# Optimization experiments

Hardware: AMD Instinct MI355X
Metric: run time of the kernel (lower is better)

## Reference

```python
import jax, jax.numpy as jnp
import numpy as np

EMBED = 384
HEADS = 6
HEAD_SIZE = EMBED // HEADS
EPS = 1e-5


def _layernorm(x, g, b):
    mu = jnp.mean(x, axis=-1, keepdims=True)
    var = jnp.mean(jnp.square(x - mu), axis=-1, keepdims=True)
    return (x - mu) * jax.lax.rsqrt(var + EPS) * g + b


def setup_inputs() -> dict:
    key = jax.random.key(0)
    ks = jax.random.split(key, 16)
    B, T = 64, 256
    s_in = 1.0 / np.sqrt(EMBED)
    return {
        "x": jax.random.normal(ks[0], (B, T, EMBED), dtype=jnp.float32),
        # per-head q/k/v projections, stacked over heads: [H, C, D]
        "Wq": jax.random.normal(ks[1], (HEADS, EMBED, HEAD_SIZE), dtype=jnp.float32) * s_in,
        "bq": jnp.zeros((HEADS, HEAD_SIZE), dtype=jnp.float32),
        "Wk": jax.random.normal(ks[2], (HEADS, EMBED, HEAD_SIZE), dtype=jnp.float32) * s_in,
        "bk": jnp.zeros((HEADS, HEAD_SIZE), dtype=jnp.float32),
        "Wv": jax.random.normal(ks[3], (HEADS, EMBED, HEAD_SIZE), dtype=jnp.float32) * s_in,
        "bv": jnp.zeros((HEADS, HEAD_SIZE), dtype=jnp.float32),
        "Wp": jax.random.normal(ks[4], (EMBED, EMBED), dtype=jnp.float32) * s_in,
        "bp": jnp.zeros((EMBED,), dtype=jnp.float32),
        "W1": jax.random.normal(ks[5], (EMBED, EMBED), dtype=jnp.float32) * s_in,
        "b1": jnp.zeros((EMBED,), dtype=jnp.float32),
        "W2": jax.random.normal(ks[6], (EMBED, EMBED), dtype=jnp.float32) * s_in,
        "b2": jnp.zeros((EMBED,), dtype=jnp.float32),
        "ln1_g": jnp.ones((EMBED,), dtype=jnp.float32),
        "ln1_b": jnp.zeros((EMBED,), dtype=jnp.float32),
        "ln2_g": jnp.ones((EMBED,), dtype=jnp.float32),
        "ln2_b": jnp.zeros((EMBED,), dtype=jnp.float32),
    }


def reference(x, Wq, bq, Wk, bk, Wv, bv, Wp, bp, W1, b1, W2, b2,
              ln1_g, ln1_b, ln2_g, ln2_b):
    B, T, C = x.shape
    h = _layernorm(x, ln1_g, ln1_b)
    # batched per-head projections: [B,H,T,D]
    q = jnp.einsum('btc,hcd->bhtd', h, Wq) + bq[None, :, None, :]
    k = jnp.einsum('btc,hcd->bhtd', h, Wk) + bk[None, :, None, :]
    v = jnp.einsum('btc,hcd->bhtd', h, Wv) + bv[None, :, None, :]
    # NOTE: original scales by embed_size**0.5 (C=384), not head_size.
    wei = jnp.einsum('bhtd,bhsd->bhts', q, k) / jnp.sqrt(jnp.float32(C))
    causal = jnp.tril(jnp.ones((T, T), dtype=bool))
    wei = jnp.where(causal[None, None], wei, -jnp.inf)
    wei = jax.nn.softmax(wei, axis=-1)  # dropout = identity in eval
    attn = jnp.einsum('bhts,bhsd->bhtd', wei, v)  # [B,H,T,D]
    # concat heads in head order -> [B,T,C]
    attn = attn.transpose(0, 2, 1, 3).reshape(B, T, C)
    x = x + attn @ Wp + bp
    h2 = _layernorm(x, ln2_g, ln2_b)
    ff = jax.nn.relu(h2 @ W1 + b1) @ W2 + b2
    return x + ff
```

## Files before the change

kernel.cpp:

```cpp
#include <hip/hip_runtime.h>

typedef _Float16 f16;
typedef _Float16 half8 __attribute__((ext_vector_type(8)));
typedef _Float16 half4v __attribute__((ext_vector_type(4)));
typedef float floatx4 __attribute__((ext_vector_type(4)));

#define B_ 64
#define T_ 256
#define C_ 384
#define H_ 6
#define D_ 64
#define NROWS (B_*T_)

typedef __attribute__((address_space(3))) void lds_void_t;
typedef const __attribute__((address_space(1))) void gvoid_t;

__device__ __forceinline__ void g2lds16(const void* g, void* l) {
  __builtin_amdgcn_global_load_lds((gvoid_t*)g, (lds_void_t*)l, 16, 0, 0);
}

__global__ __launch_bounds__(256) void prep_ln_kernel(
    const float* __restrict__ Wq, const float* __restrict__ Wk, const float* __restrict__ Wv,
    const float* __restrict__ bq, const float* __restrict__ bk, const float* __restrict__ bv,
    const float* __restrict__ Wp, const float* __restrict__ W1, const float* __restrict__ W2,
    f16* __restrict__ Wqkv_t, f16* __restrict__ Wp_t, f16* __restrict__ W1_t, f16* __restrict__ W2_t,
    float* __restrict__ bqkv,
    const float* __restrict__ x, const float* __restrict__ gamma, const float* __restrict__ beta,
    f16* __restrict__ hout)
{
  const int bid = blockIdx.x;
  const int tid = threadIdx.x;
  if (bid >= 217) {
    int row = (bid - 217) * 4 + (tid >> 6);
    int lane = tid & 63;
    const float* xr = x + (size_t)row * 384;
    float v[6]; float s = 0.f;
#pragma unroll
    for (int j = 0; j < 6; j++) { v[j] = xr[lane + 64*j]; s += v[j]; }
#pragma unroll
    for (int m = 1; m < 64; m <<= 1) s += __shfl_xor(s, m);
    float mu = s * (1.f/384.f);
    float var = 0.f;
#pragma unroll
    for (int j = 0; j < 6; j++) { float d = v[j]-mu; var += d*d; }
#pragma unroll
    for (int m = 1; m < 64; m <<= 1) var += __shfl_xor(var, m);
    float rs = rsqrtf(var * (1.f/384.f) + 1e-5f);
    f16* orow = hout + (size_t)row*384;
#pragma unroll
    for (int j = 0; j < 6; j++) {
      int col = lane + 64*j;
      orow[col] = (f16)((v[j]-mu)*rs*gamma[col] + beta[col]);
    }
    return;
  }
  if (bid == 216) {
    for (int i = tid; i < 1152; i += 256) {
      float v;
      if (i < 384)      v = bq[i];
      else if (i < 768) v = bk[i - 384];
      else              v = bv[i - 768];
      bqkv[i] = v;
    }
    return;
  }
  __shared__ __align__(16) float tile[64*68];
  const float* src; int srcStride; f16* dst;
  if (bid < 108) {
    int mat = bid / 36, rem = bid - mat*36;
    int h = rem / 6, kt = rem - h*6;
    const float* W = (mat == 0) ? Wq : (mat == 1) ? Wk : Wv;
    src = W + (size_t)(h*384 + kt*64)*64;
    srcStride = 64;
    dst = Wqkv_t + (size_t)(mat*384 + h*64)*384 + kt*64;
  } else {
    int b2 = bid - 108;
    int mat = b2 / 36, rem = b2 - mat*36;
    int kt = rem / 6, ct = rem - kt*6;
    const float* W = (mat == 0) ? Wp : (mat == 1) ? W1 : W2;
    src = W + (size_t)(kt*64)*384 + ct*64;
    srcStride = 384;
    f16* O = (mat == 0) ? Wp_t : (mat == 1) ? W1_t : W2_t;
    dst = O + (size_t)(ct*64)*384 + kt*64;
  }
#pragma unroll
  for (int i = 0; i < 4; i++) {
    int idx = i*256 + tid;
    int r = idx >> 4, c4 = idx & 15;
    float4 v = *(const float4*)(src + (size_t)r*srcStride + c4*4);
    *(float4*)(&tile[r*68 + c4*4]) = v;
  }
  __syncthreads();
#pragma unroll
  for (int i = 0; i < 4; i++) {
    int idx = i*256 + tid;
    int d = idx >> 4, k4 = idx & 15;
    half4v o;
#pragma unroll
    for (int j = 0; j < 4; j++) o[j] = (f16)tile[(k4*4 + j)*68 + d];
    *(half4v*)(dst + (size_t)d*384 + k4*4) = o;
  }
}

__global__ __launch_bounds__(256) void ln_kernel(const float* __restrict__ x,
    const float* __restrict__ gamma, const float* __restrict__ beta, f16* __restrict__ out)
{
  int row = blockIdx.x * 4 + (threadIdx.x >> 6);
  int lane = threadIdx.x & 63;
  const float* xr = x + (size_t)row * 384;
  float v[6]; float s = 0.f;
#pragma unroll
  for (int j = 0; j < 6; j++) { v[j] = xr[lane + 64*j]; s += v[j]; }
#pragma unroll
  for (int m = 1; m < 64; m <<= 1) s += __shfl_xor(s, m);
  float mu = s * (1.f/384.f);
  float var = 0.f;
#pragma unroll
  for (int j = 0; j < 6; j++) { float d = v[j]-mu; var += d*d; }
#pragma unroll
  for (int m = 1; m < 64; m <<= 1) var += __shfl_xor(var, m);
  float rs = rsqrtf(var * (1.f/384.f) + 1e-5f);
  f16* orow = out + (size_t)row*384;
#pragma unroll
  for (int j = 0; j < 6; j++) {
    int col = lane + 64*j;
    orow[col] = (f16)((v[j]-mu)*rs*gamma[col] + beta[col]);
  }
}

template<int MODE>
__global__ __launch_bounds__(256) void gemm_kernel(
    const f16* __restrict__ A, const f16* __restrict__ Bt,
    const float* __restrict__ bias, const float* __restrict__ res,
    void* __restrict__ outp, int ldo)
{
  __shared__ __align__(16) f16 As[2][128*32];
  __shared__ __align__(16) f16 Bs[2][128*32];
  const int tid = threadIdx.x;
  const int lane = tid & 63, w = tid >> 6;
  const int wm = w >> 1, wn = w & 1;
  const int q = lane >> 4, c15 = lane & 15;
  const long row0 = (long)blockIdx.x * 128;
  const long col0 = (long)blockIdx.y * 128;
  floatx4 acc[4][4] = {};

  const int c0 = tid,        r0c = c0 >> 2, p0 = c0 & 3, g0 = p0 ^ ((r0c >> 1) & 3);
  const int c1 = 256 + tid,  r1c = c1 >> 2, p1 = c1 & 3, g1 = p1 ^ ((r1c >> 1) & 3);
  const f16* Arow0 = A  + (row0 + r0c)*384 + g0*8;
  const f16* Arow1 = A  + (row0 + r1c)*384 + g1*8;
  const f16* Brow0 = Bt + (col0 + r0c)*384 + g0*8;
  const f16* Brow1 = Bt + (col0 + r1c)*384 + g1*8;
  const int dof0 = (w*64)*8, dof1 = (256 + w*64)*8;

  for (int k0 = 0; k0 < 384; k0 += 64) {
#pragma unroll
    for (int hf = 0; hf < 2; hf++) {
      int kk = k0 + hf*32;
      g2lds16(Arow0 + kk, &As[hf][dof0]);
      g2lds16(Arow1 + kk, &As[hf][dof1]);
      g2lds16(Brow0 + kk, &Bs[hf][dof0]);
      g2lds16(Brow1 + kk, &Bs[hf][dof1]);
    }
    __syncthreads();
#pragma unroll
    for (int hf = 0; hf < 2; hf++) {
      half8 af[4], bf[4];
#pragma unroll
      for (int mi = 0; mi < 4; mi++) {
        int r = wm*64 + mi*16 + c15;
        int ph = q ^ ((r >> 1) & 3);
        af[mi] = *(const half8*)(&As[hf][r*32 + ph*8]);
      }
#pragma unroll
      for (int ni = 0; ni < 4; ni++) {
        int r = wn*64 + ni*16 + c15;
        int ph = q ^ ((r >> 1) & 3);
        bf[ni] = *(const half8*)(&Bs[hf][r*32 + ph*8]);
      }
#pragma unroll
      for (int mi = 0; mi < 4; mi++)
#pragma unroll
        for (int ni = 0; ni < 4; ni++)
          acc[mi][ni] = __builtin_amdgcn_mfma_f32_16x16x32_f16(af[mi], bf[ni], acc[mi][ni], 0, 0, 0);
    }
    __syncthreads();
  }

#pragma unroll
  for (int ni = 0; ni < 4; ni++) {
    long col = col0 + wn*64 + ni*16 + c15;
    float bv = bias[col];
#pragma unroll
    for (int mi = 0; mi < 4; mi++) {
      long rowb = row0 + wm*64 + mi*16 + q*4;
#pragma unroll
      for (int r = 0; r < 4; r++) {
        float vo = acc[mi][ni][r] + bv;
        if (MODE == 1) vo = vo > 0.f ? vo : 0.f;
        long o = (rowb + r) * (long)ldo + col;
        if (MODE == 2) {
          ((float*)outp)[o] = vo + res[o];
        } else {
          ((f16*)outp)[o] = (f16)vo;
        }
      }
    }
  }
}

__global__ __launch_bounds__(256, 3) void attn_kernel(const f16* __restrict__ qkv,
                                                      f16* __restrict__ attn_out)
{
  __shared__ __align__(16) char kvbuf[32768];
  __shared__ __align__(16) f16 Pbuf[4][16*128];
  f16* Ks = (f16*)kvbuf;
  unsigned int* vTw = (unsigned int*)kvbuf;
  f16* vT = (f16*)kvbuf;

  const int tid = threadIdx.x;
  const int bid = blockIdx.x;
  const int bh = bid >> 2, qt = bid & 3;
  const int b = bh / 6, h = bh - b*6;
  const f16* qp = qkv + (size_t)b*256*1152 + h*64;
  const f16* kp = qp + 384;
  const f16* vp = qp + 768;
  const int lane = tid & 63, w = tid >> 6;
  const int q = lane >> 4, c15 = lane & 15;

  {
    const int iters = (qt + 1) * 2;
    const int pcbase = w*64 + lane;
    for (int i = 0; i < iters; i++) {
      int pc = i*256 + pcbase;
      int rc = pc >> 3, p = pc & 7;
      int c = p ^ (rc & 7);
      g2lds16(kp + (size_t)rc*1152 + c*8, (char*)kvbuf + (size_t)(i*256 + w*64)*16);
    }
  }
  __syncthreads();

  const int nmax = qt*4 + w;
  const int trow0 = qt*64 + w*16;
  const f16* qrow = qp + (size_t)(trow0 + c15)*1152 + q*8;
  half8 aq0 = *(const half8*)(qrow);
  half8 aq1 = *(const half8*)(qrow + 32);

  floatx4 sacc[16];
#pragma unroll
  for (int ni = 0; ni < 16; ni++) {
    if (ni <= nmax) {
      int s = ni*16 + c15;
      const f16* kr = Ks + s*64;
      int p0 = q ^ (s & 7);
      half8 b0 = *(const half8*)(kr + p0*8);
      half8 b1 = *(const half8*)(kr + (p0 ^ 4)*8);
      floatx4 a = {0.f, 0.f, 0.f, 0.f};
      a = __builtin_amdgcn_mfma_f32_16x16x32_f16(aq0, b0, a, 0, 0, 0);
      a = __builtin_amdgcn_mfma_f32_16x16x32_f16(aq1, b1, a, 0, 0, 0);
      sacc[ni] = a;
    }
  }

  const float scale = 0.051031036307982884f;
  float mx[4] = {-1e30f, -1e30f, -1e30f, -1e30f};
#pragma unroll
  for (int ni = 0; ni < 16; ni++) {
    if (ni < nmax) {
#pragma unroll
      for (int r = 0; r < 4; r++) { float v = sacc[ni][r]*scale; sacc[ni][r] = v; mx[r] = fmaxf(mx[r], v); }
    } else if (ni == nmax) {
#pragma unroll
      for (int r = 0; r < 4; r++) {
        float v = sacc[ni][r]*scale;
        v = (c15 <= q*4 + r) ? v : -1e30f;
        sacc[ni][r] = v; mx[r] = fmaxf(mx[r], v);
      }
    }
  }
#pragma unroll
  for (int r = 0; r < 4; r++) {
    mx[r] = fmaxf(mx[r], __shfl_xor(mx[r], 1));
    mx[r] = fmaxf(mx[r], __shfl_xor(mx[r], 2));
    mx[r] = fmaxf(mx[r], __shfl_xor(mx[r], 4));
    mx[r] = fmaxf(mx[r], __shfl_xor(mx[r], 8));
  }
  float l[4] = {0.f, 0.f, 0.f, 0.f};
#pragma unroll
  for (int ni = 0; ni < 16; ni++) {
    if (ni <= nmax) {
#pragma unroll
      for (int r = 0; r < 4; r++) { float p = __expf(sacc[ni][r] - mx[r]); sacc[ni][r] = p; l[r] += p; }
    }
  }
#pragma unroll
  for (int r = 0; r < 4; r++) {
    l[r] += __shfl_xor(l[r], 1);
    l[r] += __shfl_xor(l[r], 2);
    l[r] += __shfl_xor(l[r], 4);
    l[r] += __shfl_xor(l[r], 8);
  }
  __syncthreads();

  {
    const int iters = qt + 1;
    for (int i = 0; i < iters; i++) {
      int idx = i*256 + tid;
      int sp = idx >> 3, part = idx & 7;
      const f16* v0 = vp + (size_t)(2*sp)*1152 + part*8;
      half8 va = *(const half8*)(v0);
      half8 vb = *(const half8*)(v0 + 1152);
      int csp = sp >> 2, spw = sp & 3;
#pragma unroll
      for (int j = 0; j < 8; j++) {
        int d = part*8 + j;
        int swz = (d & 15) ^ (d >> 3);
        int p = csp ^ swz;
        union { struct { f16 lo, hi; } s; unsigned int u; } pk;
        pk.s.lo = va[j]; pk.s.hi = vb[j];
        vTw[d*128 + p*4 + spw] = pk.u;
      }
    }
  }
  __syncthreads();

  f16* Pw = &Pbuf[w][0];
  floatx4 oacc[4] = {};
  const int kend_w = (nmax + 1) * 16;
#pragma unroll
  for (int ch = 0; ch < 2; ch++) {
    if (ch*128 < kend_w) {
#pragma unroll
      for (int nl = 0; nl < 8; nl++) {
        int ni = ch*8 + nl;
        if (ni <= nmax) {
#pragma unroll
          for (int r = 0; r < 4; r++) {
            int row = q*4 + r;
            int colp = nl*16 + c15;
            int php = (colp >> 3) ^ row;
            Pw[row*128 + php*8 + (colp & 7)] = (f16)sacc[ni][r];
          }
        } else if (ni == nmax + 1) {
#pragma unroll
          for (int r = 0; r < 4; r++) {
            int row = q*4 + r;
            int colp = nl*16 + c15;
            int php = (colp >> 3) ^ row;
            Pw[row*128 + php*8 + (colp & 7)] = (f16)0.f;
          }
        }
      }
#pragma unroll
      for (int kc = 0; kc < 4; kc++) {
        if (ch*128 + kc*32 < kend_w) {
          int pc = (kc*4 + q) ^ c15;
          half8 ap = *(const half8*)(Pw + c15*128 + pc*8);
          int sc = ch*16 + kc*4 + q;
#pragma unroll
          for (int nt = 0; nt < 4; nt++) {
            int d = nt*16 + c15;
            int swz = (d & 15) ^ (d >> 3);
            half8 bv = *(const half8*)(vT + d*256 + ((sc ^ swz))*8);
            oacc[nt] = __builtin_amdgcn_mfma_f32_16x16x32_f16(ap, bv, oacc[nt], 0, 0, 0);
          }
        }
      }
    }
  }

#pragma unroll
  for (int nt = 0; nt < 4; nt++) {
#pragma unroll
    for (int r = 0; r < 4; r++) {
      int t = trow0 + q*4 + r;
      int d = nt*16 + c15;
      attn_out[(size_t)(b*256 + t)*384 + h*64 + d] = (f16)(oacc[nt][r] / l[r]);
    }
  }
}

extern "C" void kernel_launch(void* const* d_in, const int* in_sizes, int n_in,
                              void* d_out, int out_size, void* d_ws, size_t ws_size,
                              hipStream_t stream) {
  const float* x   = (const float*)d_in[0];
  const float* Wq  = (const float*)d_in[1];
  const float* bq  = (const float*)d_in[2];
  const float* Wk  = (const float*)d_in[3];
  const float* bk  = (const float*)d_in[4];
  const float* Wv  = (const float*)d_in[5];
  const float* bv  = (const float*)d_in[6];
  const float* Wp  = (const float*)d_in[7];
  const float* bp  = (const float*)d_in[8];
  const float* W1  = (const float*)d_in[9];
  const float* b1  = (const float*)d_in[10];
  const float* W2  = (const float*)d_in[11];
  const float* b2  = (const float*)d_in[12];
  const float* g1  = (const float*)d_in[13];
  const float* be1 = (const float*)d_in[14];
  const float* g2  = (const float*)d_in[15];
  const float* be2 = (const float*)d_in[16];

  char* ws = (char*)d_ws;
  size_t off = 0;
  auto alloc = [&](size_t bytes) -> void* {
    void* p = ws + off;
    off += (bytes + 255) & ~(size_t)255;
    return p;
  };
  f16*   Wqkv_t = (f16*)  alloc(1152*384*sizeof(f16));
  f16*   Wp_t   = (f16*)  alloc(384*384*sizeof(f16));
  f16*   W1_t   = (f16*)  alloc(384*384*sizeof(f16));
  f16*   W2_t   = (f16*)  alloc(384*384*sizeof(f16));
  float* bqkv   = (float*)alloc(1152*sizeof(float));
  f16*   h      = (f16*)  alloc((size_t)NROWS*384*sizeof(f16));
  f16*   qkv    = (f16*)  alloc((size_t)NROWS*1152*sizeof(f16));
  f16*   attnb  = (f16*)  alloc((size_t)NROWS*384*sizeof(f16));
  float* x2     = (float*)alloc((size_t)NROWS*384*sizeof(float));
  f16*   h2     = (f16*)  alloc((size_t)NROWS*384*sizeof(f16));
  f16*   mid    = (f16*)  alloc((size_t)NROWS*384*sizeof(f16));

  prep_ln_kernel<<<217 + NROWS/4, 256, 0, stream>>>(Wq, Wk, Wv, bq, bk, bv, Wp, W1, W2,
                                                    Wqkv_t, Wp_t, W1_t, W2_t, bqkv,
                                                    x, g1, be1, h);
  gemm_kernel<0><<<dim3(128, 9), 256, 0, stream>>>(h, Wqkv_t, bqkv, nullptr, qkv, 1152);
  attn_kernel<<<B_*H_*4, 256, 0, stream>>>(qkv, attnb);
  gemm_kernel<2><<<dim3(128, 3), 256, 0, stream>>>(attnb, Wp_t, bp, x, x2, 384);
  ln_kernel<<<NROWS/4, 256, 0, stream>>>(x2, g2, be2, h2);
  gemm_kernel<1><<<dim3(128, 3), 256, 0, stream>>>(h2, W1_t, b1, nullptr, mid, 384);
  gemm_kernel<2><<<dim3(128, 3), 256, 0, stream>>>(mid, W2_t, b2, x2, (float*)d_out, 384);
}
```

Before: 204.6 us.

## Fuse output projection with LayerNorm2 and fuse both FFN GEMMs via LDS

Replaces the separate projection GEMM, LN kernel and two FFN GEMMs with two kernels that each own full 64x384 row tiles. The projection kernel adds bias and residual, then computes LayerNorm in registers. The FFN kernel keeps the ReLU intermediate in LDS and feeds it straight into the second GEMM. This removes the round trips of mid and x2 through global memory plus two launches. In exchange, only 256 blocks run, one per CU by launch bounds, each with large LDS use and a big accumulator array, so occupancy and latency hiding drop and the B tiles are reloaded per block.

Result: slower. 220.5 us (+7.8%).

```diff
diff --git a/kernel.cpp b/kernel.cpp
--- a/kernel.cpp
+++ b/kernel.cpp
@@ -102,37 +102,9 @@
   }
 }
 
-__global__ __launch_bounds__(256) void ln_kernel(const float* __restrict__ x,
-    const float* __restrict__ gamma, const float* __restrict__ beta, f16* __restrict__ out)
-{
-  int row = blockIdx.x * 4 + (threadIdx.x >> 6);
-  int lane = threadIdx.x & 63;
-  const float* xr = x + (size_t)row * 384;
-  float v[6]; float s = 0.f;
-#pragma unroll
-  for (int j = 0; j < 6; j++) { v[j] = xr[lane + 64*j]; s += v[j]; }
-#pragma unroll
-  for (int m = 1; m < 64; m <<= 1) s += __shfl_xor(s, m);
-  float mu = s * (1.f/384.f);
-  float var = 0.f;
-#pragma unroll
-  for (int j = 0; j < 6; j++) { float d = v[j]-mu; var += d*d; }
-#pragma unroll
-  for (int m = 1; m < 64; m <<= 1) var += __shfl_xor(var, m);
-  float rs = rsqrtf(var * (1.f/384.f) + 1e-5f);
-  f16* orow = out + (size_t)row*384;
-#pragma unroll
-  for (int j = 0; j < 6; j++) {
-    int col = lane + 64*j;
-    orow[col] = (f16)((v[j]-mu)*rs*gamma[col] + beta[col]);
-  }
-}
-
-template<int MODE>
-__global__ __launch_bounds__(256) void gemm_kernel(
+__global__ __launch_bounds__(256) void gemm_qkv_kernel(
     const f16* __restrict__ A, const f16* __restrict__ Bt,
-    const float* __restrict__ bias, const float* __restrict__ res,
-    void* __restrict__ outp, int ldo)
+    const float* __restrict__ bias, f16* __restrict__ outp, int ldo)
 {
   __shared__ __align__(16) f16 As[2][128*32];
   __shared__ __align__(16) f16 Bs[2][128*32];
@@ -195,15 +167,210 @@
       long rowb = row0 + wm*64 + mi*16 + q*4;
 #pragma unroll
       for (int r = 0; r < 4; r++) {
-        float vo = acc[mi][ni][r] + bv;
-        if (MODE == 1) vo = vo > 0.f ? vo : 0.f;
-        long o = (rowb + r) * (long)ldo + col;
-        if (MODE == 2) {
-          ((float*)outp)[o] = vo + res[o];
-        } else {
-          ((f16*)outp)[o] = (f16)vo;
+        outp[(rowb + r) * (long)ldo + col] = (f16)(acc[mi][ni][r] + bv);
+      }
+    }
+  }
+}
+
+__global__ __launch_bounds__(256, 1) void projln_kernel(
+    const f16* __restrict__ A, const f16* __restrict__ Bt, const float* __restrict__ bias,
+    const float* __restrict__ res, const float* __restrict__ g2v, const float* __restrict__ be2,
+    float* __restrict__ x2, f16* __restrict__ h2)
+{
+  __shared__ __align__(16) f16 As2[2][64*32];
+  __shared__ __align__(16) f16 Bs2[2][384*32];
+  const int tid = threadIdx.x;
+  const int lane = tid & 63, w = tid >> 6;
+  const int q = lane >> 4, c15 = lane & 15;
+  const long row0 = (long)blockIdx.x * 64;
+  floatx4 acc[24] = {};
+
+  const int rcA = tid >> 2, pA = tid & 3, gA = pA ^ ((rcA >> 1) & 3);
+  const f16* Asrc = A + (row0 + rcA)*384 + gA*8;
+
+  for (int k0 = 0; k0 < 384; k0 += 64) {
+#pragma unroll
+    for (int hf = 0; hf < 2; hf++) {
+      int kk = k0 + hf*32;
+      g2lds16(Asrc + kk, &As2[hf][(w*64)*8]);
+#pragma unroll
+      for (int i = 0; i < 6; i++) {
+        int pc = i*256 + tid;
+        int rcB = pc >> 2, pB = pc & 3, gB = pB ^ ((rcB >> 1) & 3);
+        g2lds16(Bt + (size_t)rcB*384 + kk + gB*8, &Bs2[hf][(i*256 + w*64)*8]);
+      }
+    }
+    __syncthreads();
+#pragma unroll
+    for (int hf = 0; hf < 2; hf++) {
+      int ra = w*16 + c15;
+      int pha = q ^ ((ra >> 1) & 3);
+      half8 af = *(const half8*)(&As2[hf][ra*32 + pha*8]);
+#pragma unroll
+      for (int nt = 0; nt < 24; nt++) {
+        int rb = nt*16 + c15;
+        int phb = q ^ ((rb >> 1) & 3);
+        half8 bf = *(const half8*)(&Bs2[hf][rb*32 + phb*8]);
+        acc[nt] = __builtin_amdgcn_mfma_f32_16x16x32_f16(af, bf, acc[nt], 0, 0, 0);
+      }
+    }
+    __syncthreads();
+  }
+
+  const long rowg = row0 + w*16 + q*4;
+#pragma unroll
+  for (int nt = 0; nt < 24; nt++) {
+    int col = nt*16 + c15;
+    float bv = bias[col];
+#pragma unroll
+    for (int r = 0; r < 4; r++) {
+      float v = acc[nt][r] + bv + res[(rowg + r)*384 + col];
+      acc[nt][r] = v;
+      x2[(rowg + r)*384 + col] = v;
+    }
+  }
+  float s[4] = {0.f, 0.f, 0.f, 0.f};
+#pragma unroll
+  for (int nt = 0; nt < 24; nt++)
+#pragma unroll
+    for (int r = 0; r < 4; r++) s[r] += acc[nt][r];
+#pragma unroll
+  for (int r = 0; r < 4; r++) {
+    s[r] += __shfl_xor(s[r], 1);
+    s[r] += __shfl_xor(s[r], 2);
+    s[r] += __shfl_xor(s[r], 4);
+    s[r] += __shfl_xor(s[r], 8);
+  }
+  float mu[4], vs[4] = {0.f, 0.f, 0.f, 0.f};
+#pragma unroll
+  for (int r = 0; r < 4; r++) mu[r] = s[r] * (1.f/384.f);
+#pragma unroll
+  for (int nt = 0; nt < 24; nt++)
+#pragma unroll
+    for (int r = 0; r < 4; r++) { float d = acc[nt][r] - mu[r]; vs[r] += d*d; }
+#pragma unroll
+  for (int r = 0; r < 4; r++) {
+    vs[r] += __shfl_xor(vs[r], 1);
+    vs[r] += __shfl_xor(vs[r], 2);
+    vs[r] += __shfl_xor(vs[r], 4);
+    vs[r] += __shfl_xor(vs[r], 8);
+  }
+  float rs[4];
+#pragma unroll
+  for (int r = 0; r < 4; r++) rs[r] = rsqrtf(vs[r] * (1.f/384.f) + 1e-5f);
+#pragma unroll
+  for (int nt = 0; nt < 24; nt++) {
+    int col = nt*16 + c15;
+    float gg = g2v[col], bb = be2[col];
+#pragma unroll
+    for (int r = 0; r < 4; r++) {
+      h2[(rowg + r)*384 + col] = (f16)((acc[nt][r] - mu[r])*rs[r]*gg + bb);
+    }
+  }
+}
+
+__global__ __launch_bounds__(256, 1) void ffn_kernel(
+    const f16* __restrict__ h2, const f16* __restrict__ W1t, const float* __restrict__ b1,
+    const f16* __restrict__ W2t, const float* __restrict__ b2,
+    const float* __restrict__ x2, float* __restrict__ outp)
+{
+  __shared__ __align__(16) f16 As2[2][64*32];
+  __shared__ __align__(16) f16 Bs2[2][384*32];
+  __shared__ __align__(16) f16 midb[64*384];
+  const int tid = threadIdx.x;
+  const int lane = tid & 63, w = tid >> 6;
+  const int q = lane >> 4, c15 = lane & 15;
+  const long row0 = (long)blockIdx.x * 64;
+
+  const int rcA = tid >> 2, pA = tid & 3, gA = pA ^ ((rcA >> 1) & 3);
+  const f16* Asrc = h2 + (row0 + rcA)*384 + gA*8;
+
+  {
+    floatx4 acc[24] = {};
+    for (int k0 = 0; k0 < 384; k0 += 64) {
+#pragma unroll
+      for (int hf = 0; hf < 2; hf++) {
+        int kk = k0 + hf*32;
+        g2lds16(Asrc + kk, &As2[hf][(w*64)*8]);
+#pragma unroll
+        for (int i = 0; i < 6; i++) {
+          int pc = i*256 + tid;
+          int rcB = pc >> 2, pB = pc & 3, gB = pB ^ ((rcB >> 1) & 3);
+          g2lds16(W1t + (size_t)rcB*384 + kk + gB*8, &Bs2[hf][(i*256 + w*64)*8]);
         }
       }
+      __syncthreads();
+#pragma unroll
+      for (int hf = 0; hf < 2; hf++) {
+        int ra = w*16 + c15;
+        int pha = q ^ ((ra >> 1) & 3);
+        half8 af = *(const half8*)(&As2[hf][ra*32 + pha*8]);
+#pragma unroll
+        for (int nt = 0; nt < 24; nt++) {
+          int rb = nt*16 + c15;
+          int phb = q ^ ((rb >> 1) & 3);
+          half8 bf = *(const half8*)(&Bs2[hf][rb*32 + phb*8]);
+          acc[nt] = __builtin_amdgcn_mfma_f32_16x16x32_f16(af, bf, acc[nt], 0, 0, 0);
+        }
+      }
+      __syncthreads();
+    }
+#pragma unroll
+    for (int nt = 0; nt < 24; nt++) {
+      int col = nt*16 + c15;
+      float bv = b1[col];
+#pragma unroll
+      for (int r = 0; r < 4; r++) {
+        float v = acc[nt][r] + bv;
+        v = v > 0.f ? v : 0.f;
+        int row = w*16 + q*4 + r;
+        int chunk = col >> 3;
+        int ph = chunk ^ (row & 7);
+        midb[row*384 + ph*8 + (col & 7)] = (f16)v;
+      }
+    }
+  }
+  __syncthreads();
+
+  floatx4 acc2[24] = {};
+  for (int k0 = 0; k0 < 384; k0 += 64) {
+#pragma unroll
+    for (int hf = 0; hf < 2; hf++) {
+      int kk = k0 + hf*32;
+#pragma unroll
+      for (int i = 0; i < 6; i++) {
+        int pc = i*256 + tid;
+        int rcB = pc >> 2, pB = pc & 3, gB = pB ^ ((rcB >> 1) & 3);
+        g2lds16(W2t + (size_t)rcB*384 + kk + gB*8, &Bs2[hf][(i*256 + w*64)*8]);
+      }
+    }
+    __syncthreads();
+#pragma unroll
+    for (int hf = 0; hf < 2; hf++) {
+      int row = w*16 + c15;
+      int chunk = (k0 >> 3) + hf*4 + q;
+      int ph = chunk ^ (row & 7);
+      half8 af = *(const half8*)(&midb[row*384 + ph*8]);
+#pragma unroll
+      for (int nt = 0; nt < 24; nt++) {
+        int rb = nt*16 + c15;
+        int phb = q ^ ((rb >> 1) & 3);
+        half8 bf = *(const half8*)(&Bs2[hf][rb*32 + phb*8]);
+        acc2[nt] = __builtin_amdgcn_mfma_f32_16x16x32_f16(af, bf, acc2[nt], 0, 0, 0);
+      }
+    }
+    __syncthreads();
+  }
+  const long rowg = row0 + w*16 + q*4;
+#pragma unroll
+  for (int nt = 0; nt < 24; nt++) {
+    int col = nt*16 + c15;
+    float bv = b2[col];
+#pragma unroll
+    for (int r = 0; r < 4; r++) {
+      long o = (rowg + r)*384 + col;
+      outp[o] = acc2[nt][r] + bv + x2[o];
     }
   }
 }
@@ -417,15 +584,12 @@
   f16*   attnb  = (f16*)  alloc((size_t)NROWS*384*sizeof(f16));
   float* x2     = (float*)alloc((size_t)NROWS*384*sizeof(float));
   f16*   h2     = (f16*)  alloc((size_t)NROWS*384*sizeof(f16));
-  f16*   mid    = (f16*)  alloc((size_t)NROWS*384*sizeof(f16));
 
   prep_ln_kernel<<<217 + NROWS/4, 256, 0, stream>>>(Wq, Wk, Wv, bq, bk, bv, Wp, W1, W2,
                                                     Wqkv_t, Wp_t, W1_t, W2_t, bqkv,
                                                     x, g1, be1, h);
-  gemm_kernel<0><<<dim3(128, 9), 256, 0, stream>>>(h, Wqkv_t, bqkv, nullptr, qkv, 1152);
+  gemm_qkv_kernel<<<dim3(128, 9), 256, 0, stream>>>(h, Wqkv_t, bqkv, qkv, 1152);
   attn_kernel<<<B_*H_*4, 256, 0, stream>>>(qkv, attnb);
-  gemm_kernel<2><<<dim3(128, 3), 256, 0, stream>>>(attnb, Wp_t, bp, x, x2, 384);
-  ln_kernel<<<NROWS/4, 256, 0, stream>>>(x2, g2, be2, h2);
-  gemm_kernel<1><<<dim3(128, 3), 256, 0, stream>>>(h2, W1_t, b1, nullptr, mid, 384);
-  gemm_kernel<2><<<dim3(128, 3), 256, 0, stream>>>(mid, W2_t, b2, x2, (float*)d_out, 384);
-}
+  projln_kernel<<<NROWS/64, 256, 0, stream>>>(attnb, Wp_t, bp, x, g2, be2, x2, h2);
+  ffn_kernel<<<NROWS/64, 256, 0, stream>>>(h2, W1_t, b1, W2_t, b2, x2, (float*)d_out);
+}
```

## Fuse output projection with LayerNorm2 and retile FFN GEMMs to 128x64

Applied to the files above, without the earlier changes.

Replaces the separate projection GEMM and LayerNorm kernels with one kernel. Each block computes full 384-wide rows for 32 rows, adds bias and residual, and reduces the row statistics in registers and shared memory to write both x2 and h2. This removes a launch and a full re-read of x2. The FFN GEMMs switch to 128x64 tiles, doubling the grid from 384 to 768 blocks to fill more CUs. In exchange, each projection block reloads all of Wp, has fewer MFMA tiles per LDS load, and computes variance as E[x^2]-mu^2, which is less numerically robust.

Result: no change. 208.2 us (+1.7%).

```diff
diff --git a/kernel.cpp b/kernel.cpp
--- a/kernel.cpp
+++ b/kernel.cpp
@@ -102,37 +102,9 @@
   }
 }
 
-__global__ __launch_bounds__(256) void ln_kernel(const float* __restrict__ x,
-    const float* __restrict__ gamma, const float* __restrict__ beta, f16* __restrict__ out)
-{
-  int row = blockIdx.x * 4 + (threadIdx.x >> 6);
-  int lane = threadIdx.x & 63;
-  const float* xr = x + (size_t)row * 384;
-  float v[6]; float s = 0.f;
-#pragma unroll
-  for (int j = 0; j < 6; j++) { v[j] = xr[lane + 64*j]; s += v[j]; }
-#pragma unroll
-  for (int m = 1; m < 64; m <<= 1) s += __shfl_xor(s, m);
-  float mu = s * (1.f/384.f);
-  float var = 0.f;
-#pragma unroll
-  for (int j = 0; j < 6; j++) { float d = v[j]-mu; var += d*d; }
-#pragma unroll
-  for (int m = 1; m < 64; m <<= 1) var += __shfl_xor(var, m);
-  float rs = rsqrtf(var * (1.f/384.f) + 1e-5f);
-  f16* orow = out + (size_t)row*384;
-#pragma unroll
-  for (int j = 0; j < 6; j++) {
-    int col = lane + 64*j;
-    orow[col] = (f16)((v[j]-mu)*rs*gamma[col] + beta[col]);
-  }
-}
-
-template<int MODE>
-__global__ __launch_bounds__(256) void gemm_kernel(
+__global__ __launch_bounds__(256) void gemm_qkv_kernel(
     const f16* __restrict__ A, const f16* __restrict__ Bt,
-    const float* __restrict__ bias, const float* __restrict__ res,
-    void* __restrict__ outp, int ldo)
+    const float* __restrict__ bias, f16* __restrict__ outp, int ldo)
 {
   __shared__ __align__(16) f16 As[2][128*32];
   __shared__ __align__(16) f16 Bs[2][128*32];
@@ -195,14 +167,206 @@
       long rowb = row0 + wm*64 + mi*16 + q*4;
 #pragma unroll
       for (int r = 0; r < 4; r++) {
+        outp[(rowb + r) * (long)ldo + col] = (f16)(acc[mi][ni][r] + bv);
+      }
+    }
+  }
+}
+
+template<int MODE>
+__global__ __launch_bounds__(256) void gemm64_kernel(
+    const f16* __restrict__ A, const f16* __restrict__ Bt,
+    const float* __restrict__ bias, const float* __restrict__ res,
+    void* __restrict__ outp)
+{
+  __shared__ __align__(16) f16 As[2][128*32];
+  __shared__ __align__(16) f16 Bs[2][64*32];
+  const int tid = threadIdx.x;
+  const int lane = tid & 63, w = tid >> 6;
+  const int wm = w >> 1, wn = w & 1;
+  const int q = lane >> 4, c15 = lane & 15;
+  const long row0 = (long)blockIdx.x * 128;
+  const long col0 = (long)blockIdx.y * 64;
+  floatx4 acc[4][2] = {};
+
+  const int cA0 = tid,       rA0 = cA0 >> 2, pA0 = cA0 & 3, gA0 = pA0 ^ ((rA0 >> 1) & 3);
+  const int cA1 = 256 + tid, rA1 = cA1 >> 2, pA1 = cA1 & 3, gA1 = pA1 ^ ((rA1 >> 1) & 3);
+  const int rB  = tid >> 2,  pB  = tid & 3,  gB  = pB ^ ((rB >> 1) & 3);
+  const f16* Arow0 = A  + (row0 + rA0)*384 + gA0*8;
+  const f16* Arow1 = A  + (row0 + rA1)*384 + gA1*8;
+  const f16* Brow  = Bt + (col0 + rB)*384 + gB*8;
+  const int dofA0 = (w*64)*8, dofA1 = (256 + w*64)*8, dofB = (w*64)*8;
+
+  for (int k0 = 0; k0 < 384; k0 += 64) {
+#pragma unroll
+    for (int hf = 0; hf < 2; hf++) {
+      int kk = k0 + hf*32;
+      g2lds16(Arow0 + kk, &As[hf][dofA0]);
+      g2lds16(Arow1 + kk, &As[hf][dofA1]);
+      g2lds16(Brow + kk, &Bs[hf][dofB]);
+    }
+    __syncthreads();
+#pragma unroll
+    for (int hf = 0; hf < 2; hf++) {
+      half8 af[4], bf[2];
+#pragma unroll
+      for (int mi = 0; mi < 4; mi++) {
+        int r = wm*64 + mi*16 + c15;
+        int ph = q ^ ((r >> 1) & 3);
+        af[mi] = *(const half8*)(&As[hf][r*32 + ph*8]);
+      }
+#pragma unroll
+      for (int ni = 0; ni < 2; ni++) {
+        int r = wn*32 + ni*16 + c15;
+        int ph = q ^ ((r >> 1) & 3);
+        bf[ni] = *(const half8*)(&Bs[hf][r*32 + ph*8]);
+      }
+#pragma unroll
+      for (int mi = 0; mi < 4; mi++)
+#pragma unroll
+        for (int ni = 0; ni < 2; ni++)
+          acc[mi][ni] = __builtin_amdgcn_mfma_f32_16x16x32_f16(af[mi], bf[ni], acc[mi][ni], 0, 0, 0);
+    }
+    __syncthreads();
+  }
+
+#pragma unroll
+  for (int ni = 0; ni < 2; ni++) {
+    long col = col0 + wn*32 + ni*16 + c15;
+    float bv = bias[col];
+#pragma unroll
+    for (int mi = 0; mi < 4; mi++) {
+      long rowb = row0 + wm*64 + mi*16 + q*4;
+#pragma unroll
+      for (int r = 0; r < 4; r++) {
         float vo = acc[mi][ni][r] + bv;
-        if (MODE == 1) vo = vo > 0.f ? vo : 0.f;
-        long o = (rowb + r) * (long)ldo + col;
-        if (MODE == 2) {
+        long o = (rowb + r) * 384 + col;
+        if (MODE == 1) {
+          vo = vo > 0.f ? vo : 0.f;
+          ((f16*)outp)[o] = (f16)vo;
+        } else {
           ((float*)outp)[o] = vo + res[o];
-        } else {
-          ((f16*)outp)[o] = (f16)vo;
         }
+      }
+    }
+  }
+}
+
+__global__ __launch_bounds__(256, 2) void projln2_kernel(
+    const f16* __restrict__ A, const f16* __restrict__ Bt, const float* __restrict__ bias,
+    const float* __restrict__ res, const float* __restrict__ g2v, const float* __restrict__ be2,
+    float* __restrict__ x2, f16* __restrict__ h2)
+{
+  __shared__ __align__(16) f16 As2[2][32*32];
+  __shared__ __align__(16) f16 Bs2[2][384*32];
+  __shared__ float redS[4][32], redS2[4][32];
+  const int tid = threadIdx.x;
+  const int lane = tid & 63, w = tid >> 6;
+  const int q = lane >> 4, c15 = lane & 15;
+  const long row0 = (long)blockIdx.x * 32;
+  floatx4 acc[2][6] = {};
+
+  const int hfA = w >> 1;
+  const int idxA = (w & 1)*64 + lane;
+  const int rA = idxA >> 2, pA = idxA & 3, gA = pA ^ ((rA >> 1) & 3);
+  const f16* Asrc = A + (row0 + rA)*384 + hfA*32 + gA*8;
+  f16* Adst = &As2[hfA][((w & 1)*64)*8];
+
+  for (int k0 = 0; k0 < 384; k0 += 64) {
+    g2lds16(Asrc + k0, Adst);
+#pragma unroll
+    for (int hf = 0; hf < 2; hf++) {
+#pragma unroll
+      for (int i = 0; i < 6; i++) {
+        int pc = i*256 + tid;
+        int rc = pc >> 2, p = pc & 3, g = p ^ ((rc >> 1) & 3);
+        g2lds16(Bt + (size_t)rc*384 + k0 + hf*32 + g*8, &Bs2[hf][(i*256 + w*64)*8]);
+      }
+    }
+    __syncthreads();
+#pragma unroll
+    for (int hf = 0; hf < 2; hf++) {
+      half8 af[2], bf[6];
+#pragma unroll
+      for (int mi = 0; mi < 2; mi++) {
+        int r = mi*16 + c15;
+        int ph = q ^ ((r >> 1) & 3);
+        af[mi] = *(const half8*)(&As2[hf][r*32 + ph*8]);
+      }
+#pragma unroll
+      for (int j = 0; j < 6; j++) {
+        int rb = (w*6 + j)*16 + c15;
+        int ph = q ^ ((rb >> 1) & 3);
+        bf[j] = *(const half8*)(&Bs2[hf][rb*32 + ph*8]);
+      }
+#pragma unroll
+      for (int mi = 0; mi < 2; mi++)
+#pragma unroll
+        for (int j = 0; j < 6; j++)
+          acc[mi][j] = __builtin_amdgcn_mfma_f32_16x16x32_f16(af[mi], bf[j], acc[mi][j], 0, 0, 0);
+    }
+    __syncthreads();
+  }
+
+  float s[8] = {}, s2[8] = {};
+#pragma unroll
+  for (int mi = 0; mi < 2; mi++) {
+#pragma unroll
+    for (int j = 0; j < 6; j++) {
+      int col = (w*6 + j)*16 + c15;
+      float bv = bias[col];
+#pragma unroll
+      for (int r = 0; r < 4; r++) {
+        long rowg = row0 + mi*16 + q*4 + r;
+        float v = acc[mi][j][r] + bv + res[rowg*384 + col];
+        acc[mi][j][r] = v;
+        x2[rowg*384 + col] = v;
+        s[mi*4 + r] += v;
+        s2[mi*4 + r] += v*v;
+      }
+    }
+  }
+#pragma unroll
+  for (int i = 0; i < 8; i++) {
+#pragma unroll
+    for (int m = 1; m <= 8; m <<= 1) {
+      s[i]  += __shfl_xor(s[i], m);
+      s2[i] += __shfl_xor(s2[i], m);
+    }
+  }
+  if (c15 == 0) {
+#pragma unroll
+    for (int mi = 0; mi < 2; mi++)
+#pragma unroll
+      for (int r = 0; r < 4; r++) {
+        redS[w][mi*16 + q*4 + r]  = s[mi*4 + r];
+        redS2[w][mi*16 + q*4 + r] = s2[mi*4 + r];
+      }
+  }
+  __syncthreads();
+  float mu[8], rs[8];
+#pragma unroll
+  for (int mi = 0; mi < 2; mi++)
+#pragma unroll
+    for (int r = 0; r < 4; r++) {
+      int row = mi*16 + q*4 + r;
+      float S  = redS[0][row] + redS[1][row] + redS[2][row] + redS[3][row];
+      float S2 = redS2[0][row] + redS2[1][row] + redS2[2][row] + redS2[3][row];
+      float m_ = S * (1.f/384.f);
+      float var = S2 * (1.f/384.f) - m_*m_;
+      mu[mi*4 + r] = m_;
+      rs[mi*4 + r] = rsqrtf(var + 1e-5f);
+    }
+#pragma unroll
+  for (int mi = 0; mi < 2; mi++) {
+#pragma unroll
+    for (int j = 0; j < 6; j++) {
+      int col = (w*6 + j)*16 + c15;
+      float gg = g2v[col], bb = be2[col];
+#pragma unroll
+      for (int r = 0; r < 4; r++) {
+        long rowg = row0 + mi*16 + q*4 + r;
+        h2[rowg*384 + col] = (f16)((acc[mi][j][r] - mu[mi*4 + r])*rs[mi*4 + r]*gg + bb);
       }
     }
   }
@@ -422,10 +586,9 @@
   prep_ln_kernel<<<217 + NROWS/4, 256, 0, stream>>>(Wq, Wk, Wv, bq, bk, bv, Wp, W1, W2,
                                                     Wqkv_t, Wp_t, W1_t, W2_t, bqkv,
                                                     x, g1, be1, h);
-  gemm_kernel<0><<<dim3(128, 9), 256, 0, stream>>>(h, Wqkv_t, bqkv, nullptr, qkv, 1152);
+  gemm_qkv_kernel<<<dim3(128, 9), 256, 0, stream>>>(h, Wqkv_t, bqkv, qkv, 1152);
   attn_kernel<<<B_*H_*4, 256, 0, stream>>>(qkv, attnb);
-  gemm_kernel<2><<<dim3(128, 3), 256, 0, stream>>>(attnb, Wp_t, bp, x, x2, 384);
-  ln_kernel<<<NROWS/4, 256, 0, stream>>>(x2, g2, be2, h2);
-  gemm_kernel<1><<<dim3(128, 3), 256, 0, stream>>>(h2, W1_t, b1, nullptr, mid, 384);
-  gemm_kernel<2><<<dim3(128, 3), 256, 0, stream>>>(mid, W2_t, b2, x2, (float*)d_out, 384);
-}
+  projln2_kernel<<<NROWS/32, 256, 0, stream>>>(attnb, Wp_t, bp, x, g2, be2, x2, h2);
+  gemm64_kernel<1><<<dim3(128, 6), 256, 0, stream>>>(h2, W1_t, b1, nullptr, mid);
+  gemm64_kernel<2><<<dim3(128, 6), 256, 0, stream>>>(mid, W2_t, b2, x2, (float*)d_out);
+}
```

## Split causal attention scores into two chunks with online softmax rescaling

Applied to the files above, without the earlier changes.

The attention kernel now computes QK^T scores in two 128-column chunks instead of holding all 16 score tiles in registers. It uses an online-softmax update (running max, alpha rescale of the row sum and output accumulator) to merge the chunks. The first chunk's probabilities are written to LDS before the barrier and reused by the PV pass, and the second chunk is processed afterwards. This halves the score accumulator register footprint, which may allow higher occupancy, at the cost of extra exp/rescale work and more control flow for later query tiles.

Result: slower. 343.9 us (+68.1%).

```diff
diff --git a/kernel.cpp b/kernel.cpp
--- a/kernel.cpp
+++ b/kernel.cpp
@@ -240,15 +240,22 @@
   __syncthreads();
 
   const int nmax = qt*4 + w;
+  const int n0max = nmax < 7 ? nmax : 7;
   const int trow0 = qt*64 + w*16;
   const f16* qrow = qp + (size_t)(trow0 + c15)*1152 + q*8;
   half8 aq0 = *(const half8*)(qrow);
   half8 aq1 = *(const half8*)(qrow + 32);
-
-  floatx4 sacc[16];
-#pragma unroll
-  for (int ni = 0; ni < 16; ni++) {
-    if (ni <= nmax) {
+  const float scale = 0.051031036307982884f;
+  f16* Pw = &Pbuf[w][0];
+
+  floatx4 sacc[8];
+  float mx[4] = {-1e30f, -1e30f, -1e30f, -1e30f};
+  float l[4] = {0.f, 0.f, 0.f, 0.f};
+  float alpha[4] = {1.f, 1.f, 1.f, 1.f};
+
+#pragma unroll
+  for (int ni = 0; ni < 8; ni++) {
+    if (ni <= n0max) {
       int s = ni*16 + c15;
       const f16* kr = Ks + s*64;
       int p0 = q ^ (s & 7);
@@ -260,12 +267,9 @@
       sacc[ni] = a;
     }
   }
-
-  const float scale = 0.051031036307982884f;
-  float mx[4] = {-1e30f, -1e30f, -1e30f, -1e30f};
-#pragma unroll
-  for (int ni = 0; ni < 16; ni++) {
-    if (ni < nmax) {
+#pragma unroll
+  for (int ni = 0; ni < 8; ni++) {
+    if (ni < nmax && ni <= n0max) {
 #pragma unroll
       for (int r = 0; r < 4; r++) { float v = sacc[ni][r]*scale; sacc[ni][r] = v; mx[r] = fmaxf(mx[r], v); }
     } else if (ni == nmax) {
@@ -284,10 +288,9 @@
     mx[r] = fmaxf(mx[r], __shfl_xor(mx[r], 4));
     mx[r] = fmaxf(mx[r], __shfl_xor(mx[r], 8));
   }
-  float l[4] = {0.f, 0.f, 0.f, 0.f};
-#pragma unroll
-  for (int ni = 0; ni < 16; ni++) {
-    if (ni <= nmax) {
+#pragma unroll
+  for (int ni = 0; ni < 8; ni++) {
+    if (ni <= n0max) {
 #pragma unroll
       for (int r = 0; r < 4; r++) { float p = __expf(sacc[ni][r] - mx[r]); sacc[ni][r] = p; l[r] += p; }
     }
@@ -298,6 +301,87 @@
     l[r] += __shfl_xor(l[r], 2);
     l[r] += __shfl_xor(l[r], 4);
     l[r] += __shfl_xor(l[r], 8);
+  }
+#pragma unroll
+  for (int nl = 0; nl < 8; nl++) {
+    if (nl <= n0max) {
+#pragma unroll
+      for (int r = 0; r < 4; r++) {
+        int row = q*4 + r;
+        int colp = nl*16 + c15;
+        int php = (colp >> 3) ^ row;
+        Pw[row*128 + php*8 + (colp & 7)] = (f16)sacc[nl][r];
+      }
+    } else if (nl == n0max + 1) {
+#pragma unroll
+      for (int r = 0; r < 4; r++) {
+        int row = q*4 + r;
+        int colp = nl*16 + c15;
+        int php = (colp >> 3) ^ row;
+        Pw[row*128 + php*8 + (colp & 7)] = (f16)0.f;
+      }
+    }
+  }
+
+  if (nmax >= 8) {
+#pragma unroll
+    for (int ni = 8; ni < 16; ni++) {
+      if (ni <= nmax) {
+        int s = ni*16 + c15;
+        const f16* kr = Ks + s*64;
+        int p0 = q ^ (s & 7);
+        half8 b0 = *(const half8*)(kr + p0*8);
+        half8 b1 = *(const half8*)(kr + (p0 ^ 4)*8);
+        floatx4 a = {0.f, 0.f, 0.f, 0.f};
+        a = __builtin_amdgcn_mfma_f32_16x16x32_f16(aq0, b0, a, 0, 0, 0);
+        a = __builtin_amdgcn_mfma_f32_16x16x32_f16(aq1, b1, a, 0, 0, 0);
+        sacc[ni - 8] = a;
+      }
+    }
+    float cm[4] = {-1e30f, -1e30f, -1e30f, -1e30f};
+#pragma unroll
+    for (int ni = 8; ni < 16; ni++) {
+      if (ni < nmax) {
+#pragma unroll
+        for (int r = 0; r < 4; r++) { float v = sacc[ni-8][r]*scale; sacc[ni-8][r] = v; cm[r] = fmaxf(cm[r], v); }
+      } else if (ni == nmax) {
+#pragma unroll
+        for (int r = 0; r < 4; r++) {
+          float v = sacc[ni-8][r]*scale;
+          v = (c15 <= q*4 + r) ? v : -1e30f;
+          sacc[ni-8][r] = v; cm[r] = fmaxf(cm[r], v);
+        }
+      }
+    }
+#pragma unroll
+    for (int r = 0; r < 4; r++) {
+      cm[r] = fmaxf(cm[r], __shfl_xor(cm[r], 1));
+      cm[r] = fmaxf(cm[r], __shfl_xor(cm[r], 2));
+      cm[r] = fmaxf(cm[r], __shfl_xor(cm[r], 4));
+      cm[r] = fmaxf(cm[r], __shfl_xor(cm[r], 8));
+    }
+    float l1[4] = {0.f, 0.f, 0.f, 0.f};
+#pragma unroll
+    for (int r = 0; r < 4; r++) {
+      float mn = fmaxf(mx[r], cm[r]);
+      alpha[r] = __expf(mx[r] - mn);
+      mx[r] = mn;
+    }
+#pragma unroll
+    for (int ni = 8; ni < 16; ni++) {
+      if (ni <= nmax) {
+#pragma unroll
+        for (int r = 0; r < 4; r++) { float p = __expf(sacc[ni-8][r] - mx[r]); sacc[ni-8][r] = p; l1[r] += p; }
+      }
+    }
+#pragma unroll
+    for (int r = 0; r < 4; r++) {
+      l1[r] += __shfl_xor(l1[r], 1);
+      l1[r] += __shfl_xor(l1[r], 2);
+      l1[r] += __shfl_xor(l1[r], 4);
+      l1[r] += __shfl_xor(l1[r], 8);
+      l[r] = l[r]*alpha[r] + l1[r];
+    }
   }
   __syncthreads();
 
@@ -323,46 +407,62 @@
   }
   __syncthreads();
 
-  f16* Pw = &Pbuf[w][0];
   floatx4 oacc[4] = {};
   const int kend_w = (nmax + 1) * 16;
 #pragma unroll
-  for (int ch = 0; ch < 2; ch++) {
-    if (ch*128 < kend_w) {
-#pragma unroll
-      for (int nl = 0; nl < 8; nl++) {
-        int ni = ch*8 + nl;
-        if (ni <= nmax) {
-#pragma unroll
-          for (int r = 0; r < 4; r++) {
-            int row = q*4 + r;
-            int colp = nl*16 + c15;
-            int php = (colp >> 3) ^ row;
-            Pw[row*128 + php*8 + (colp & 7)] = (f16)sacc[ni][r];
-          }
-        } else if (ni == nmax + 1) {
-#pragma unroll
-          for (int r = 0; r < 4; r++) {
-            int row = q*4 + r;
-            int colp = nl*16 + c15;
-            int php = (colp >> 3) ^ row;
-            Pw[row*128 + php*8 + (colp & 7)] = (f16)0.f;
-          }
+  for (int kc = 0; kc < 4; kc++) {
+    if (kc*32 < kend_w) {
+      int pc = (kc*4 + q) ^ c15;
+      half8 ap = *(const half8*)(Pw + c15*128 + pc*8);
+      int sc = kc*4 + q;
+#pragma unroll
+      for (int nt = 0; nt < 4; nt++) {
+        int d = nt*16 + c15;
+        int swz = (d & 15) ^ (d >> 3);
+        half8 bv = *(const half8*)(vT + d*256 + ((sc ^ swz))*8);
+        oacc[nt] = __builtin_amdgcn_mfma_f32_16x16x32_f16(ap, bv, oacc[nt], 0, 0, 0);
+      }
+    }
+  }
+
+  if (nmax >= 8) {
+#pragma unroll
+    for (int nt = 0; nt < 4; nt++)
+#pragma unroll
+      for (int r = 0; r < 4; r++) oacc[nt][r] *= alpha[r];
+#pragma unroll
+    for (int nl = 0; nl < 8; nl++) {
+      int ni = 8 + nl;
+      if (ni <= nmax) {
+#pragma unroll
+        for (int r = 0; r < 4; r++) {
+          int row = q*4 + r;
+          int colp = nl*16 + c15;
+          int php = (colp >> 3) ^ row;
+          Pw[row*128 + php*8 + (colp & 7)] = (f16)sacc[nl][r];
         }
-      }
-#pragma unroll
-      for (int kc = 0; kc < 4; kc++) {
-        if (ch*128 + kc*32 < kend_w) {
-          int pc = (kc*4 + q) ^ c15;
-          half8 ap = *(const half8*)(Pw + c15*128 + pc*8);
-          int sc = ch*16 + kc*4 + q;
-#pragma unroll
-          for (int nt = 0; nt < 4; nt++) {
-            int d = nt*16 + c15;
-            int swz = (d & 15) ^ (d >> 3);
-            half8 bv = *(const half8*)(vT + d*256 + ((sc ^ swz))*8);
-            oacc[nt] = __builtin_amdgcn_mfma_f32_16x16x32_f16(ap, bv, oacc[nt], 0, 0, 0);
-          }
+      } else if (ni == nmax + 1) {
+#pragma unroll
+        for (int r = 0; r < 4; r++) {
+          int row = q*4 + r;
+          int colp = nl*16 + c15;
+          int php = (colp >> 3) ^ row;
+          Pw[row*128 + php*8 + (colp & 7)] = (f16)0.f;
+        }
+      }
+    }
+#pragma unroll
+    for (int kc = 0; kc < 4; kc++) {
+      if (128 + kc*32 < kend_w) {
+        int pc = (kc*4 + q) ^ c15;
+        half8 ap = *(const half8*)(Pw + c15*128 + pc*8);
+        int sc = 16 + kc*4 + q;
+#pragma unroll
+        for (int nt = 0; nt < 4; nt++) {
+          int d = nt*16 + c15;
+          int swz = (d & 15) ^ (d >> 3);
+          half8 bv = *(const half8*)(vT + d*256 + ((sc ^ swz))*8);
+          oacc[nt] = __builtin_amdgcn_mfma_f32_16x16x32_f16(ap, bv, oacc[nt], 0, 0, 0);
         }
       }
     }
```
